# Performance work log

Hardware: AMD Instinct MI355X
Metric: run time of the kernel (lower is better)

Reference implementation:

```python
import jax, jax.numpy as jnp
import numpy as np
from functools import partial

B, D, E, O, K = 65536, 64, 16, 512, 2  # batch, feat dim, num_experts, output_size, top-k


def setup_inputs() -> dict:
    key = jax.random.key(0)
    k1, k2, k3, k4, k5 = jax.random.split(key, 5)
    scale_g = 1.0 / np.sqrt(D)
    return {
        "x": jax.random.normal(k1, (B, D), dtype=jnp.float32),
        "wg": jax.random.uniform(k2, (D, E), dtype=jnp.float32, minval=-scale_g, maxval=scale_g),
        "bg": jnp.zeros((E,), dtype=jnp.float32),
        "We": jax.random.uniform(k3, (E, D, O), dtype=jnp.float32, minval=-scale_g, maxval=scale_g),
        "be": jax.random.uniform(k4, (E, O), dtype=jnp.float32, minval=-scale_g, maxval=scale_g),
    }


def reference(x, wg, bg, We, be):
    # --- gating (noisy_gating=False / eval path) ---
    logits = jax.nn.softmax(x @ wg + bg, axis=1)            # [B, E]
    top_vals, top_idx = jax.lax.top_k(logits, K)            # [B, K]
    top_gates = top_vals / (jnp.sum(top_vals, axis=1, keepdims=True) + 1e-6)
    rows = jnp.arange(x.shape[0])[:, None]                  # [B, 1]
    gates = jnp.zeros_like(logits).at[rows, top_idx].set(top_gates)  # dense [B, E], sparse rows

    # --- dispatch / per-expert linear / gated scatter-combine ---
    # Equivalent dense-masked form of SparseDispatcher: y[i] = sum_e gates[i,e] * (x[i] @ We[e] + be[e])
    def step(y, ewb):
        w, b, g = ewb                                       # [D,O], [O], [B]
        return y + g[:, None] * (x @ w + b), None

    y0 = jnp.zeros((x.shape[0], We.shape[2]), dtype=x.dtype)
    y, _ = jax.lax.scan(step, y0, (We, be, gates.T))
    return y
```

## Files before the change

### kernel.cpp

```cpp
#include <hip/hip_runtime.h>

typedef unsigned int u32;
typedef unsigned short u16;
typedef float f4 __attribute__((ext_vector_type(4)));
typedef __bf16 b8 __attribute__((ext_vector_type(8)));
typedef unsigned short us8 __attribute__((ext_vector_type(8)));

#define DD 64
#define NE 16
#define OO 512
#define TR 64

struct __align__(16) Tile { u32 pid, slot, nr, pad; };

union U8 { us8 u; b8 b; };

__device__ __forceinline__ u16 f2bf(float f) {
  u32 u = __float_as_uint(f);
  u32 r = (u + 0x7fffu + ((u >> 16) & 1u)) >> 16;
  return (u16)r;
}

__global__ void k_wt(const float* __restrict__ We, u16* __restrict__ WeT) {
  __shared__ float tl[64][65];
  int b = blockIdx.x;
  int e = b >> 3;
  int oc = (b & 7) * 64;
  int t = threadIdx.x;
  int d = t >> 2, seg = (t & 3) * 16;
  const f4* src = (const f4*)(We + ((size_t)(e * DD + d)) * OO + oc + seg);
  f4 v0 = src[0], v1 = src[1], v2 = src[2], v3 = src[3];
#pragma unroll
  for (int j = 0; j < 4; j++) {
    tl[d][seg + j]      = v0[j];
    tl[d][seg + 4 + j]  = v1[j];
    tl[d][seg + 8 + j]  = v2[j];
    tl[d][seg + 12 + j] = v3[j];
  }
  __syncthreads();
  int o = t >> 2, ds = (t & 3) * 16;
  us8 o0, o1;
#pragma unroll
  for (int j = 0; j < 8; j++) {
    o0[j] = f2bf(tl[ds + j][o]);
    o1[j] = f2bf(tl[ds + 8 + j][o]);
  }
  u16* dst = WeT + ((size_t)(e * OO + oc + o)) * DD + ds;
  *(us8*)dst = o0;
  *(us8*)(dst + 8) = o1;
}

__global__ void k_gate(const float* __restrict__ x, const float* __restrict__ wg,
                       const float* __restrict__ bg, u32* __restrict__ hist,
                       u32* __restrict__ pid_arr, float* __restrict__ glo_arr,
                       float* __restrict__ ghi_arr) {
  __shared__ u32 hcnt[256];
  int t = threadIdx.x;
  hcnt[t] = 0;
  __syncthreads();
  int row = blockIdx.x * 256 + t;

  float l[NE];
#pragma unroll
  for (int e = 0; e < NE; e++) l[e] = bg[e];

  const f4* xp = (const f4*)(x + (size_t)row * DD);
  for (int d4 = 0; d4 < 16; d4++) {
    f4 xv = xp[d4];
#pragma unroll
    for (int qq = 0; qq < 4; qq++) {
      float xs = xv[qq];
      const float* wrow = wg + (d4 * 4 + qq) * NE;
#pragma unroll
      for (int e = 0; e < NE; e++) l[e] = fmaf(xs, wrow[e], l[e]);
    }
  }
  float mx = l[0];
#pragma unroll
  for (int e = 1; e < NE; e++) mx = fmaxf(mx, l[e]);
  float Z = 0.f;
#pragma unroll
  for (int e = 0; e < NE; e++) Z += __expf(l[e] - mx);
  int i1 = 0; float b1 = l[0];
#pragma unroll
  for (int e = 1; e < NE; e++) { if (l[e] > b1) { b1 = l[e]; i1 = e; } }
  int i2 = -1; float b2 = -1e30f;
#pragma unroll
  for (int e = 0; e < NE; e++) { if (e != i1 && l[e] > b2) { b2 = l[e]; i2 = e; } }
  float p1 = __expf(b1 - mx) / Z;
  float p2 = __expf(b2 - mx) / Z;
  float den = p1 + p2 + 1e-6f;
  float g1 = p1 / den, g2 = p2 / den;
  int elo, ehi; float glo, ghi;
  if (i1 < i2) { elo = i1; ehi = i2; glo = g1; ghi = g2; }
  else         { elo = i2; ehi = i1; glo = g2; ghi = g1; }
  u32 pid = (u32)(elo * NE + ehi);
  pid_arr[row] = pid;
  glo_arr[row] = glo;
  ghi_arr[row] = ghi;
  atomicAdd(&hcnt[pid], 1u);
  __syncthreads();
  hist[blockIdx.x * 256 + t] = hcnt[t];
}

__global__ void k_colscan(u32* __restrict__ hist, u32* __restrict__ tot) {
  __shared__ u32 s[256];
  int b = threadIdx.x, p = blockIdx.x;
  u32 v = hist[b * 256 + p];
  s[b] = v;
  __syncthreads();
  for (int d = 1; d < 256; d <<= 1) {
    u32 a = 0;
    if (b >= d) a = s[b - d];
    __syncthreads();
    s[b] += a;
    __syncthreads();
  }
  hist[b * 256 + p] = s[b] - v;
  if (b == 255) tot[p] = s[255];
}

__global__ void k_base(const u32* __restrict__ tot, u32* __restrict__ base,
                       u32* __restrict__ ntp, Tile* __restrict__ tiles) {
  __shared__ u32 s[256], s2[256];
  int t = threadIdx.x;
  u32 v = tot[t];
  u32 nt = (v + (TR - 1)) >> 6;
  s[t] = v; s2[t] = nt;
  __syncthreads();
  for (int d = 1; d < 256; d <<= 1) {
    u32 a = 0, c = 0;
    if (t >= d) { a = s[t - d]; c = s2[t - d]; }
    __syncthreads();
    s[t] += a; s2[t] += c;
    __syncthreads();
  }
  u32 rb = s[t] - v;
  u32 tb = s2[t] - nt;
  base[t] = rb;
  for (u32 k = 0; k < nt; k++) {
    Tile td;
    td.pid = (u32)t;
    td.slot = rb + k * (u32)TR;
    u32 rem = v - k * (u32)TR;
    td.nr = rem < (u32)TR ? rem : (u32)TR;
    td.pad = 0;
    tiles[tb + k] = td;
  }
  if (t == 255) *ntp = s2[255];
}

__global__ void k_scatter(const u32* __restrict__ pid_arr, const u32* __restrict__ hist,
                          const u32* __restrict__ base, u32* __restrict__ sorted) {
  __shared__ u32 lcnt[256], lbase[256];
  int t = threadIdx.x;
  lcnt[t] = 0;
  lbase[t] = base[t];
  __syncthreads();
  int row = blockIdx.x * 256 + t;
  u32 pid = pid_arr[row];
  u32 rank = atomicAdd(&lcnt[pid], 1u);
  u32 off = lbase[pid] + hist[blockIdx.x * 256 + pid];
  sorted[off + rank] = (u32)row;
}

__global__ void k_moe(const float* __restrict__ x, const u16* __restrict__ WeT,
                      const float* __restrict__ be, const u32* __restrict__ sorted,
                      const u32* __restrict__ ntp, const Tile* __restrict__ tiles,
                      const float* __restrict__ glo_arr, const float* __restrict__ ghi_arr,
                      float* __restrict__ y) {
  __shared__ __align__(16) u16 Xl[TR * 72];
  __shared__ __align__(16) float Yl[TR * 68];
  __shared__ u32 rid_s[TR];
  __shared__ float glo_s[TR], ghi_s[TR];

  u32 bid = blockIdx.x;
  if (bid >= *ntp) return;
  Tile td = tiles[bid];
  u32 e_lo = td.pid >> 4, e_hi = td.pid & 15u;
  u32 slot0 = td.slot, nr = td.nr;

  int t = threadIdx.x;
  if (t < TR) {
    u32 i = (u32)t;
    u32 slot = slot0 + ((i < nr) ? i : 0u);
    u32 r = sorted[slot];
    rid_s[t] = r;
    bool valid = i < nr;
    glo_s[t] = valid ? glo_arr[r] : 0.f;
    ghi_s[t] = valid ? ghi_arr[r] : 0.f;
  }
  __syncthreads();
  {
    int i = t >> 2;
    int seg = (t & 3) * 16;
    u32 r = rid_s[i];
    const f4* xp = (const f4*)(x + (size_t)r * DD + seg);
    f4 v0 = xp[0], v1 = xp[1], v2 = xp[2], v3 = xp[3];
    float vv[16] = { v0[0], v0[1], v0[2], v0[3], v1[0], v1[1], v1[2], v1[3],
                     v2[0], v2[1], v2[2], v2[3], v3[0], v3[1], v3[2], v3[3] };
    us8 o0, o1;
#pragma unroll
    for (int j = 0; j < 8; j++) { o0[j] = f2bf(vv[j]); o1[j] = f2bf(vv[8 + j]); }
    *(us8*)&Xl[i * 72 + seg] = o0;
    *(us8*)&Xl[i * 72 + seg + 8] = o1;
  }
  __syncthreads();

  int lane = t & 63;
  int w = t >> 6;
  int q = lane >> 4;
  int ln = lane & 15;

  b8 afr[4][2];
#pragma unroll
  for (int mt = 0; mt < 4; mt++)
#pragma unroll
    for (int kc = 0; kc < 2; kc++) {
      U8 tmp; tmp.u = *(const us8*)&Xl[(mt * 16 + ln) * 72 + kc * 32 + q * 8];
      afr[mt][kc] = tmp.b;
    }

  float gl[16], gh[16];
#pragma unroll
  for (int mt = 0; mt < 4; mt++)
#pragma unroll
    for (int rr = 0; rr < 4; rr++) {
      int i = mt * 16 + q * 4 + rr;
      gl[mt * 4 + rr] = glo_s[i];
      gh[mt * 4 + rr] = ghi_s[i];
    }

  const u16* wlo = WeT + (size_t)e_lo * OO * DD;
  const u16* whi = WeT + (size_t)e_hi * OO * DD;
  const f4 zero = {0.f, 0.f, 0.f, 0.f};

  for (int jj = 0; jj < 8; jj++) {
    int col = jj * 64 + w * 16 + ln;
    const us8* plo = (const us8*)(wlo + (size_t)col * DD + q * 8);
    const us8* phi = (const us8*)(whi + (size_t)col * DD + q * 8);
    U8 t0, t1, t2, t3;
    t0.u = plo[0]; t1.u = plo[4];
    t2.u = phi[0]; t3.u = phi[4];
    b8 bl0 = t0.b, bl1 = t1.b, bh0 = t2.b, bh1 = t3.b;
    float blo = be[e_lo * OO + col];
    float bhi = be[e_hi * OO + col];

    f4 aL[4], aH[4];
#pragma unroll
    for (int mt = 0; mt < 4; mt++) { aL[mt] = zero; aH[mt] = zero; }
#pragma unroll
    for (int mt = 0; mt < 4; mt++) {
      aL[mt] = __builtin_amdgcn_mfma_f32_16x16x32_bf16(afr[mt][0], bl0, aL[mt], 0, 0, 0);
      aL[mt] = __builtin_amdgcn_mfma_f32_16x16x32_bf16(afr[mt][1], bl1, aL[mt], 0, 0, 0);
      aH[mt] = __builtin_amdgcn_mfma_f32_16x16x32_bf16(afr[mt][0], bh0, aH[mt], 0, 0, 0);
      aH[mt] = __builtin_amdgcn_mfma_f32_16x16x32_bf16(afr[mt][1], bh1, aH[mt], 0, 0, 0);
    }
#pragma unroll
    for (int mt = 0; mt < 4; mt++)
#pragma unroll
      for (int rr = 0; rr < 4; rr++) {
        int i = mt * 16 + q * 4 + rr;
        int idx = mt * 4 + rr;
        float v = gl[idx] * (aL[mt][rr] + blo) + gh[idx] * (aH[mt][rr] + bhi);
        Yl[i * 68 + w * 16 + ln] = v;
      }
    __syncthreads();
    {
      int row0 = t >> 3;
      int c8 = (t & 7) * 4;
#pragma unroll
      for (int half = 0; half < 2; half++) {
        int row = half * 32 + row0;
        if ((u32)row < nr) {
          float* yp = y + (size_t)rid_s[row] * OO + jj * 64;
          const float* sp = &Yl[row * 68];
          *(f4*)(yp + c8)      = *(const f4*)(sp + c8);
          *(f4*)(yp + 32 + c8) = *(const f4*)(sp + 32 + c8);
        }
      }
    }
    __syncthreads();
  }
}

extern "C" void kernel_launch(void* const* d_in, const int* in_sizes, int n_in,
                              void* d_out, int out_size, void* d_ws, size_t ws_size,
                              hipStream_t stream) {
  const float* x  = (const float*)d_in[0];
  const float* wg = (const float*)d_in[1];
  const float* bg = (const float*)d_in[2];
  const float* We = (const float*)d_in[3];
  const float* be = (const float*)d_in[4];
  float* y = (float*)d_out;

  char* ws = (char*)d_ws;
  u32* ntp     = (u32*)(ws + 0);
  Tile* tiles  = (Tile*)(ws + 4096);
  u32* pid_arr = (u32*)(ws + 32768);
  float* glo_a = (float*)(ws + 32768 + 262144);
  float* ghi_a = (float*)(ws + 32768 + 2 * 262144);
  u32* sorted  = (u32*)(ws + 32768 + 3 * 262144);
  u16* WeT     = (u16*)(ws + 32768 + 4 * 262144);
  u32* hist    = (u32*)(ws + 32768 + 4 * 262144 + 1048576);
  u32* tot     = (u32*)(ws + 32768 + 4 * 262144 + 1048576 + 262144);
  u32* base    = (u32*)(ws + 32768 + 4 * 262144 + 1048576 + 262144 + 1024);

  k_wt<<<128, 256, 0, stream>>>(We, WeT);
  k_gate<<<256, 256, 0, stream>>>(x, wg, bg, hist, pid_arr, glo_a, ghi_a);
  k_colscan<<<256, 256, 0, stream>>>(hist, tot);
  k_base<<<1, 256, 0, stream>>>(tot, base, ntp, tiles);
  k_scatter<<<256, 256, 0, stream>>>(pid_arr, hist, base, sorted);
  k_moe<<<1144, 256, 0, stream>>>(x, WeT, be, sorted, ntp, tiles, glo_a, ghi_a, y);
}
```

Before: 193.8 us.

## Merge weight transpose with gating kernel; drop LDS staging in MoE kernel

Folds the weight-transpose kernel into the gating kernel by giving it the first 128 blocks of one combined launch, which saves a kernel launch. The MoE kernel drops shared-memory staging of X and Y. Each wave now owns 16 rows and computes them across all 512 output columns, using swapped MFMA operands so the row's output lands in registers and can be written straight to y as contiguous float4s. This removes block-wide syncs and LDS traffic. In exchange, each wave reloads the full weight columns for its own rows, so weight reads from L2 go up about fourfold per tile.

```diff
diff --git a/kernel.cpp b/kernel.cpp
--- a/kernel.cpp
+++ b/kernel.cpp
@@ -21,44 +21,47 @@
   return (u16)r;
 }
 
-__global__ void k_wt(const float* __restrict__ We, u16* __restrict__ WeT) {
-  __shared__ float tl[64][65];
-  int b = blockIdx.x;
-  int e = b >> 3;
-  int oc = (b & 7) * 64;
-  int t = threadIdx.x;
-  int d = t >> 2, seg = (t & 3) * 16;
-  const f4* src = (const f4*)(We + ((size_t)(e * DD + d)) * OO + oc + seg);
-  f4 v0 = src[0], v1 = src[1], v2 = src[2], v3 = src[3];
-#pragma unroll
-  for (int j = 0; j < 4; j++) {
-    tl[d][seg + j]      = v0[j];
-    tl[d][seg + 4 + j]  = v1[j];
-    tl[d][seg + 8 + j]  = v2[j];
-    tl[d][seg + 12 + j] = v3[j];
-  }
-  __syncthreads();
-  int o = t >> 2, ds = (t & 3) * 16;
-  us8 o0, o1;
-#pragma unroll
-  for (int j = 0; j < 8; j++) {
-    o0[j] = f2bf(tl[ds + j][o]);
-    o1[j] = f2bf(tl[ds + 8 + j][o]);
-  }
-  u16* dst = WeT + ((size_t)(e * OO + oc + o)) * DD + ds;
-  *(us8*)dst = o0;
-  *(us8*)(dst + 8) = o1;
-}
-
-__global__ void k_gate(const float* __restrict__ x, const float* __restrict__ wg,
+__global__ void k_prep(const float* __restrict__ We, u16* __restrict__ WeT,
+                       const float* __restrict__ x, const float* __restrict__ wg,
                        const float* __restrict__ bg, u32* __restrict__ hist,
                        u32* __restrict__ pid_arr, float* __restrict__ glo_arr,
                        float* __restrict__ ghi_arr) {
+  __shared__ float tl[64][65];
   __shared__ u32 hcnt[256];
   int t = threadIdx.x;
+
+  if (blockIdx.x < 128) {
+    int b = blockIdx.x;
+    int e = b >> 3;
+    int oc = (b & 7) * 64;
+    int d = t >> 2, seg = (t & 3) * 16;
+    const f4* src = (const f4*)(We + ((size_t)(e * DD + d)) * OO + oc + seg);
+    f4 v0 = src[0], v1 = src[1], v2 = src[2], v3 = src[3];
+#pragma unroll
+    for (int j = 0; j < 4; j++) {
+      tl[d][seg + j]      = v0[j];
+      tl[d][seg + 4 + j]  = v1[j];
+      tl[d][seg + 8 + j]  = v2[j];
+      tl[d][seg + 12 + j] = v3[j];
+    }
+    __syncthreads();
+    int o = t >> 2, ds = (t & 3) * 16;
+    us8 o0, o1;
+#pragma unroll
+    for (int j = 0; j < 8; j++) {
+      o0[j] = f2bf(tl[ds + j][o]);
+      o1[j] = f2bf(tl[ds + 8 + j][o]);
+    }
+    u16* dst = WeT + ((size_t)(e * OO + oc + o)) * DD + ds;
+    *(us8*)dst = o0;
+    *(us8*)(dst + 8) = o1;
+    return;
+  }
+
+  int gb = blockIdx.x - 128;
   hcnt[t] = 0;
   __syncthreads();
-  int row = blockIdx.x * 256 + t;
+  int row = gb * 256 + t;
 
   float l[NE];
 #pragma unroll
@@ -100,7 +103,7 @@
   ghi_arr[row] = ghi;
   atomicAdd(&hcnt[pid], 1u);
   __syncthreads();
-  hist[blockIdx.x * 256 + t] = hcnt[t];
+  hist[gb * 256 + t] = hcnt[t];
 }
 
 __global__ void k_colscan(u32* __restrict__ hist, u32* __restrict__ tot) {
@@ -169,11 +172,6 @@
                       const u32* __restrict__ ntp, const Tile* __restrict__ tiles,
                       const float* __restrict__ glo_arr, const float* __restrict__ ghi_arr,
                       float* __restrict__ y) {
-  __shared__ __align__(16) u16 Xl[TR * 72];
-  __shared__ __align__(16) float Yl[TR * 68];
-  __shared__ u32 rid_s[TR];
-  __shared__ float glo_s[TR], ghi_s[TR];
-
   u32 bid = blockIdx.x;
   if (bid >= *ntp) return;
   Tile td = tiles[bid];
@@ -181,106 +179,72 @@
   u32 slot0 = td.slot, nr = td.nr;
 
   int t = threadIdx.x;
-  if (t < TR) {
-    u32 i = (u32)t;
-    u32 slot = slot0 + ((i < nr) ? i : 0u);
-    u32 r = sorted[slot];
-    rid_s[t] = r;
-    bool valid = i < nr;
-    glo_s[t] = valid ? glo_arr[r] : 0.f;
-    ghi_s[t] = valid ? ghi_arr[r] : 0.f;
-  }
-  __syncthreads();
-  {
-    int i = t >> 2;
-    int seg = (t & 3) * 16;
-    u32 r = rid_s[i];
-    const f4* xp = (const f4*)(x + (size_t)r * DD + seg);
-    f4 v0 = xp[0], v1 = xp[1], v2 = xp[2], v3 = xp[3];
-    float vv[16] = { v0[0], v0[1], v0[2], v0[3], v1[0], v1[1], v1[2], v1[3],
-                     v2[0], v2[1], v2[2], v2[3], v3[0], v3[1], v3[2], v3[3] };
-    us8 o0, o1;
-#pragma unroll
-    for (int j = 0; j < 8; j++) { o0[j] = f2bf(vv[j]); o1[j] = f2bf(vv[8 + j]); }
-    *(us8*)&Xl[i * 72 + seg] = o0;
-    *(us8*)&Xl[i * 72 + seg + 8] = o1;
-  }
-  __syncthreads();
-
+  int w = t >> 6;
   int lane = t & 63;
-  int w = t >> 6;
   int q = lane >> 4;
   int ln = lane & 15;
 
-  b8 afr[4][2];
-#pragma unroll
-  for (int mt = 0; mt < 4; mt++)
-#pragma unroll
-    for (int kc = 0; kc < 2; kc++) {
-      U8 tmp; tmp.u = *(const us8*)&Xl[(mt * 16 + ln) * 72 + kc * 32 + q * 8];
-      afr[mt][kc] = tmp.b;
-    }
-
-  float gl[16], gh[16];
-#pragma unroll
-  for (int mt = 0; mt < 4; mt++)
-#pragma unroll
-    for (int rr = 0; rr < 4; rr++) {
-      int i = mt * 16 + q * 4 + rr;
-      gl[mt * 4 + rr] = glo_s[i];
-      gh[mt * 4 + rr] = ghi_s[i];
-    }
+  int i = w * 16 + ln;
+  bool valid = (u32)i < nr;
+  u32 slot = slot0 + (valid ? (u32)i : 0u);
+  u32 rid = sorted[slot];
+  float gl = valid ? glo_arr[rid] : 0.f;
+  float gh = valid ? ghi_arr[rid] : 0.f;
+
+  const float* xr = x + (size_t)rid * DD;
+  f4 xa = *(const f4*)(xr + q * 8);
+  f4 xb = *(const f4*)(xr + q * 8 + 4);
+  f4 xc = *(const f4*)(xr + 32 + q * 8);
+  f4 xd = *(const f4*)(xr + 32 + q * 8 + 4);
+  U8 bu0, bu1;
+#pragma unroll
+  for (int j = 0; j < 4; j++) {
+    bu0.u[j] = f2bf(xa[j]); bu0.u[4 + j] = f2bf(xb[j]);
+    bu1.u[j] = f2bf(xc[j]); bu1.u[4 + j] = f2bf(xd[j]);
+  }
+  b8 bf0 = bu0.b, bf1 = bu1.b;
 
   const u16* wlo = WeT + (size_t)e_lo * OO * DD;
   const u16* whi = WeT + (size_t)e_hi * OO * DD;
+  const float* bel = be + (size_t)e_lo * OO;
+  const float* beh = be + (size_t)e_hi * OO;
+  float* yrow = y + (size_t)rid * OO;
   const f4 zero = {0.f, 0.f, 0.f, 0.f};
 
-  for (int jj = 0; jj < 8; jj++) {
-    int col = jj * 64 + w * 16 + ln;
-    const us8* plo = (const us8*)(wlo + (size_t)col * DD + q * 8);
-    const us8* phi = (const us8*)(whi + (size_t)col * DD + q * 8);
-    U8 t0, t1, t2, t3;
-    t0.u = plo[0]; t1.u = plo[4];
-    t2.u = phi[0]; t3.u = phi[4];
-    b8 bl0 = t0.b, bl1 = t1.b, bh0 = t2.b, bh1 = t3.b;
-    float blo = be[e_lo * OO + col];
-    float bhi = be[e_hi * OO + col];
-
-    f4 aL[4], aH[4];
-#pragma unroll
-    for (int mt = 0; mt < 4; mt++) { aL[mt] = zero; aH[mt] = zero; }
-#pragma unroll
-    for (int mt = 0; mt < 4; mt++) {
-      aL[mt] = __builtin_amdgcn_mfma_f32_16x16x32_bf16(afr[mt][0], bl0, aL[mt], 0, 0, 0);
-      aL[mt] = __builtin_amdgcn_mfma_f32_16x16x32_bf16(afr[mt][1], bl1, aL[mt], 0, 0, 0);
-      aH[mt] = __builtin_amdgcn_mfma_f32_16x16x32_bf16(afr[mt][0], bh0, aH[mt], 0, 0, 0);
-      aH[mt] = __builtin_amdgcn_mfma_f32_16x16x32_bf16(afr[mt][1], bh1, aH[mt], 0, 0, 0);
-    }
-#pragma unroll
-    for (int mt = 0; mt < 4; mt++)
-#pragma unroll
-      for (int rr = 0; rr < 4; rr++) {
-        int i = mt * 16 + q * 4 + rr;
-        int idx = mt * 4 + rr;
-        float v = gl[idx] * (aL[mt][rr] + blo) + gh[idx] * (aH[mt][rr] + bhi);
-        Yl[i * 68 + w * 16 + ln] = v;
+#pragma unroll
+  for (int oo = 0; oo < 4; oo++) {
+#pragma unroll
+    for (int otp = 0; otp < 4; otp++) {
+      f4 vout[2];
+#pragma unroll
+      for (int h = 0; h < 2; h++) {
+        int ot = otp * 2 + h;
+        int col = oo * 128 + ot * 16 + ln;
+        const us8* pl = (const us8*)(wlo + (size_t)col * DD + q * 8);
+        const us8* ph = (const us8*)(whi + (size_t)col * DD + q * 8);
+        U8 a0, a1, a2, a3;
+        a0.u = pl[0]; a1.u = pl[4];
+        a2.u = ph[0]; a3.u = ph[4];
+        f4 aL = zero, aH = zero;
+        aL = __builtin_amdgcn_mfma_f32_16x16x32_bf16(a0.b, bf0, aL, 0, 0, 0);
+        aL = __builtin_amdgcn_mfma_f32_16x16x32_bf16(a1.b, bf1, aL, 0, 0, 0);
+        aH = __builtin_amdgcn_mfma_f32_16x16x32_bf16(a2.b, bf0, aH, 0, 0, 0);
+        aH = __builtin_amdgcn_mfma_f32_16x16x32_bf16(a3.b, bf1, aH, 0, 0, 0);
+        int c0 = oo * 128 + ot * 16 + q * 4;
+        f4 bL = *(const f4*)(bel + c0);
+        f4 bH = *(const f4*)(beh + c0);
+        f4 v;
+#pragma unroll
+        for (int rr = 0; rr < 4; rr++)
+          v[rr] = gl * (aL[rr] + bL[rr]) + gh * (aH[rr] + bH[rr]);
+        vout[h] = v;
       }
-    __syncthreads();
-    {
-      int row0 = t >> 3;
-      int c8 = (t & 7) * 4;
-#pragma unroll
-      for (int half = 0; half < 2; half++) {
-        int row = half * 32 + row0;
-        if ((u32)row < nr) {
-          float* yp = y + (size_t)rid_s[row] * OO + jj * 64;
-          const float* sp = &Yl[row * 68];
-          *(f4*)(yp + c8)      = *(const f4*)(sp + c8);
-          *(f4*)(yp + 32 + c8) = *(const f4*)(sp + 32 + c8);
-        }
+      if (valid) {
+        int c0 = oo * 128 + otp * 32 + q * 4;
+        *(f4*)(yrow + c0)      = vout[0];
+        *(f4*)(yrow + c0 + 16) = vout[1];
       }
     }
-    __syncthreads();
   }
 }
 
@@ -306,8 +270,7 @@
   u32* tot     = (u32*)(ws + 32768 + 4 * 262144 + 1048576 + 262144);
   u32* base    = (u32*)(ws + 32768 + 4 * 262144 + 1048576 + 262144 + 1024);
 
-  k_wt<<<128, 256, 0, stream>>>(We, WeT);
-  k_gate<<<256, 256, 0, stream>>>(x, wg, bg, hist, pid_arr, glo_a, ghi_a);
+  k_prep<<<384, 256, 0, stream>>>(We, WeT, x, wg, bg, hist, pid_arr, glo_a, ghi_a);
   k_colscan<<<256, 256, 0, stream>>>(hist, tot);
   k_base<<<1, 256, 0, stream>>>(tot, base, ntp, tiles);
   k_scatter<<<256, 256, 0, stream>>>(pid_arr, hist, base, sorted);
```

Result: slower. 236.3 us (+21.9%).
